# Performance work log

Measured on AMD Instinct MI355X. Metric: run time of the kernel, lower is better.

The kernel has to match this reference:

```python
import jax, jax.numpy as jnp
import numpy as np

H = 64        # hidden_size
NOISE = 16    # noise_size
DATA = 8      # data_size
WIDTH = 128   # width_size
INIT_NOISE = 8
B = 512       # batch (original vmaps per-sample __call__)
T = 1025      # saved time points; steps = T - 1


def lipswish(x):
    return 0.909 * jax.nn.silu(x)


def _mlp(x, W0, b0, W1, b1, W2, b2, act, final_act):
    h = act(x @ W0.T + b0)
    h = act(h @ W1.T + b1)
    return final_act(h @ W2.T + b2)


def _forward(ts, z0, dW, iW0, ib0, iW1, ib1, iW2, ib2,
             vW0, vb0, vW1, vb1, vW2, vb2, vscale,
             cW0, cb0, cW1, cb1, cW2, cb2, cscale, roW, rob):
    dt = ts[1] - ts[0]
    # initial MLP: default relu activation, identity final activation
    y0 = _mlp(z0, iW0, ib0, iW1, ib1, iW2, ib2, jax.nn.relu, lambda u: u)  # (B,H)
    dw = dW * jnp.sqrt(dt)  # Brownian increments per step, (T-1,B,NOISE)

    def with_t(t, y):
        return jnp.concatenate([jnp.full((y.shape[0], 1), t, y.dtype), y], axis=1)

    def drift(t, y):
        return vscale * _mlp(with_t(t, y), vW0, vb0, vW1, vb1, vW2, vb2, lipswish, jnp.tanh)

    def diff_prod(t, y, dw_t):
        g = _mlp(with_t(t, y), cW0, cb0, cW1, cb1, cW2, cb2, lipswish, jnp.tanh)
        g = cscale * g.reshape(y.shape[0], H, NOISE)
        return jnp.einsum('bhn,bn->bh', g, dw_t)

    def step(y, inp):
        # diffrax EulerHeun (Stratonovich) step
        t, dw_t = inp
        f0 = drift(t, y) * dt
        g0 = diff_prod(t, y, dw_t)
        y_prime = y + g0
        g1 = diff_prod(t, y_prime, dw_t)
        y1 = y + f0 + 0.5 * (g0 + g1)
        return y1, y1

    _, ys = jax.lax.scan(step, y0, (ts[:-1], dw))
    ys_all = jnp.concatenate([y0[None], ys], axis=0)  # (T,B,H); SaveAt(t0=True, steps=True)
    out = ys_all @ roW.T + rob                         # readout, (T,B,DATA)
    return jnp.transpose(out, (1, 0, 2))               # (B,T,DATA)


def setup_inputs():
    key = jax.random.key(0)
    ks = jax.random.split(key, 12)

    def lin(k, out_d, in_d):
        k1, k2 = jax.random.split(k)
        lim = 1.0 / np.sqrt(in_d)
        W = jax.random.uniform(k1, (out_d, in_d), jnp.float32, -lim, lim)
        b = jax.random.uniform(k2, (out_d,), jnp.float32, -lim, lim)
        return W, b

    iW0, ib0 = lin(ks[0], WIDTH, INIT_NOISE)
    iW1, ib1 = lin(ks[1], WIDTH, WIDTH)
    iW2, ib2 = lin(ks[2], H, WIDTH)
    vW0, vb0 = lin(ks[3], WIDTH, H + 1)
    vW1, vb1 = lin(ks[4], WIDTH, WIDTH)
    vW2, vb2 = lin(ks[5], H, WIDTH)
    vscale = jax.random.uniform(ks[6], (H,), jnp.float32, 0.9, 1.1)
    cW0, cb0 = lin(ks[7], WIDTH, H + 1)
    cW1, cb1 = lin(ks[8], WIDTH, WIDTH)
    cW2, cb2 = lin(ks[9], H * NOISE, WIDTH)
    cscale = jax.random.uniform(ks[10], (H, NOISE), jnp.float32, 0.9, 1.1)
    roW, rob = lin(ks[11], DATA, H)

    kz, kw = jax.random.split(jax.random.key(1))
    ts = jnp.arange(T, dtype=jnp.float32) / (T - 1)  # uniform grid on [0,1]
    z0 = jax.random.normal(kz, (B, INIT_NOISE), jnp.float32)
    dW = jax.random.normal(kw, (T - 1, B, NOISE), jnp.float32)
    return {"ts": ts, "z0": z0, "dW": dW,
            "iW0": iW0, "ib0": ib0, "iW1": iW1, "ib1": ib1, "iW2": iW2, "ib2": ib2,
            "vW0": vW0, "vb0": vb0, "vW1": vW1, "vb1": vb1, "vW2": vW2, "vb2": vb2,
            "vscale": vscale,
            "cW0": cW0, "cb0": cb0, "cW1": cW1, "cb1": cb1, "cW2": cW2, "cb2": cb2,
            "cscale": cscale, "roW": roW, "rob": rob}


def reference(ts, z0, dW, iW0, ib0, iW1, ib1, iW2, ib2,
              vW0, vb0, vW1, vb1, vW2, vb2, vscale,
              cW0, cb0, cW1, cb1, cW2, cb2, cscale, roW, rob):
    return _forward(ts, z0, dW, iW0, ib0, iW1, ib1, iW2, ib2,
                    vW0, vb0, vW1, vb1, vW2, vb2, vscale,
                    cW0, cb0, cW1, cb1, cW2, cb2, cscale, roW, rob)
```

## Files before the change

kernel.cpp:

```cpp
#include <hip/hip_runtime.h>

typedef unsigned short u16;
typedef unsigned int   u32;
typedef __attribute__((ext_vector_type(4))) unsigned int au4;
typedef __attribute__((ext_vector_type(4))) float fx4;
typedef __attribute__((ext_vector_type(8))) __bf16 bf16x8;

#define NTHREADS 512
#define NBLOCKS  256
#define BB       2
#define STEPS    1024
#define TPTS     1025
#define HDIM     64
#define NZ       16
#define WID      128
#define IND      65
#define HN       1024

__device__ __forceinline__ float bf2f(u16 v) { return __uint_as_float(((u32)v) << 16); }
__device__ __forceinline__ u16 f2bf(float f) {
    u32 u = __float_as_uint(f);
    return (u16)((u + 0x7fffu + ((u >> 16) & 1u)) >> 16);
}
__device__ __forceinline__ float lo16(u32 u) { return __uint_as_float(u << 16); }
__device__ __forceinline__ float hi16(u32 u) { return __uint_as_float(u & 0xffff0000u); }
__device__ __forceinline__ u32 pk(float a, float b) {
    return (u32)f2bf(a) | ((u32)f2bf(b) << 16);
}

__device__ __forceinline__ au4 apin(uint4 v) {
    au4 t; t.x = v.x; t.y = v.y; t.z = v.z; t.w = v.w;
    au4 r;
    asm volatile("" : "=a"(r) : "0"(t));
    return r;
}
__device__ __forceinline__ au4 ageta(au4 a) {
    au4 t;
    asm volatile("" : "=a"(t) : "0"(a));
    return t;
}

template <bool IS32>
__device__ __forceinline__ float ldf(const void* p, int i) {
    return IS32 ? ((const float*)p)[i] : bf2f(((const u16*)p)[i]);
}
template <bool IS32>
__device__ __forceinline__ u16 ldbf(const void* p, int i) {
    return IS32 ? f2bf(((const float*)p)[i]) : ((const u16*)p)[i];
}

__device__ __forceinline__ float rcpf(float x) { return __builtin_amdgcn_rcpf(x); }
__device__ __forceinline__ float lipswish(float x) {
    return 0.909f * x * rcpf(1.0f + __expf(-x));
}
__device__ __forceinline__ float tanh_fast(float x) {
    float e = __expf(2.0f * fabsf(x));
    float t = 1.0f - 2.0f * rcpf(e + 1.0f);
    return copysignf(t, x);
}
__device__ __forceinline__ void split_bf(float v, u16& hi, u16& lo) {
    hi = f2bf(v);
    lo = f2bf(v - bf2f(hi));
}

struct __align__(16) SMem {
    __align__(16) u16 bxh[BB][96],  bxl[BB][96];
    __align__(16) u16 bh1[2][4][144];
    __align__(16) u16 bh2v[4][144];
    __align__(16) u16 bh2c[4][144];
    __align__(16) u16 vW2F[4][4][64][8];
    __align__(16) float accL0[4][264];
    __align__(16) float accL2v[4][72];
    __align__(16) float accB[4][1032];
    __align__(16) float b0s[256], b1s[256], vb2[HDIM], vsc[HDIM];
    __align__(16) float cb2[HN], csc[HN];
    __align__(16) float roW[8][HDIM];
    __align__(16) float rob[8];
    __align__(16) float tsb[1028];
    __align__(16) float yb[BB][HDIM], g0b[BB][HDIM], fdt[BB][HDIM];
    __align__(16) float dwb[BB][NZ];
};

__device__ __forceinline__ bf16x8 bfrag(const u16* p) {
    return __builtin_bit_cast(bf16x8, *(const uint4*)p);
}
__device__ __forceinline__ fx4 mf1(au4 a, bf16x8 b, fx4 acc) {
    bf16x8 af = __builtin_bit_cast(bf16x8, ageta(a));
    return __builtin_amdgcn_mfma_f32_16x16x32_bf16(af, b, acc, 0, 0, 0);
}

template <bool IS32>
__device__ __forceinline__ uint4 load8(const void* src, int row, int stride, int k0, int Klim) {
    u16 e[8];
    #pragma unroll
    for (int j = 0; j < 8; ++j) {
        int k = k0 + j;
        e[j] = (k < Klim) ? ldbf<IS32>(src, row * stride + k) : (u16)0;
    }
    uint4 v;
    v.x = (u32)e[0] | ((u32)e[1] << 16);
    v.y = (u32)e[2] | ((u32)e[3] << 16);
    v.z = (u32)e[4] | ((u32)e[5] << 16);
    v.w = (u32)e[6] | ((u32)e[7] << 16);
    return v;
}

template <bool IS32>
__device__ __forceinline__ void stage_dw(SMem& sm, const uint4& d, int q, float sdt) {
    if (IS32) {
        const float* pf = (const float*)&d;
        int f = q * 4;
        #pragma unroll
        for (int k = 0; k < 4; ++k)
            sm.dwb[(f + k) >> 4][(f + k) & 15] = pf[k] * sdt;
    } else {
        int f = q * 8;
        u32 u0 = d.x, u1 = d.y, u2 = d.z, u3 = d.w;
        sm.dwb[(f    ) >> 4][(f    ) & 15] = lo16(u0) * sdt;
        sm.dwb[(f + 1) >> 4][(f + 1) & 15] = hi16(u0) * sdt;
        sm.dwb[(f + 2) >> 4][(f + 2) & 15] = lo16(u1) * sdt;
        sm.dwb[(f + 3) >> 4][(f + 3) & 15] = hi16(u1) * sdt;
        sm.dwb[(f + 4) >> 4][(f + 4) & 15] = lo16(u2) * sdt;
        sm.dwb[(f + 5) >> 4][(f + 5) & 15] = hi16(u2) * sdt;
        sm.dwb[(f + 6) >> 4][(f + 6) & 15] = lo16(u3) * sdt;
        sm.dwb[(f + 7) >> 4][(f + 7) & 15] = hi16(u3) * sdt;
    }
}

template <bool IS32>
__device__ __forceinline__ void write_out(void* out, size_t idx, const float* v8) {
    if (IS32) {
        float4 o0, o1;
        o0.x = v8[0]; o0.y = v8[1]; o0.z = v8[2]; o0.w = v8[3];
        o1.x = v8[4]; o1.y = v8[5]; o1.z = v8[6]; o1.w = v8[7];
        ((float4*)out)[idx * 2]     = o0;
        ((float4*)out)[idx * 2 + 1] = o1;
    } else {
        uint4 o;
        o.x = pk(v8[0], v8[1]);
        o.y = pk(v8[2], v8[3]);
        o.z = pk(v8[4], v8[5]);
        o.w = pk(v8[6], v8[7]);
        ((uint4*)out)[idx] = o;
    }
}

template <bool IS32>
__device__ __forceinline__ void
sde_run(SMem& sm,
        const void* ts,  const void* z0,  const void* dW,
        const void* iW0, const void* ib0, const void* iW1, const void* ib1,
        const void* iW2, const void* ib2,
        const void* vW0, const void* vb0, const void* vW1, const void* vb1,
        const void* vW2, const void* vb2, const void* vsc,
        const void* cW0, const void* cb0, const void* cW1, const void* cb1,
        const void* cW2, const void* cb2, const void* csc,
        const void* roW, const void* rob, void* out,
        int tid, int bid)
{
    const int lane = tid & 63, wv = tid >> 6;
    const int mm = lane & 15, qq = lane >> 4;
    const int nn = mm;
    const int smp = nn & 1;
    const int prt = (nn >> 1) & 1;

    au4 a0[6];
    au4 a1[8];
    au4 ab[32];
    #pragma unroll
    for (int rtl = 0; rtl < 2; ++rtl) {
        int grow = 16 * (2 * wv + rtl) + mm;
        const void* src = (grow < 128) ? vW0 : cW0;
        int r = grow & 127;
        #pragma unroll
        for (int kt = 0; kt < 3; ++kt)
            a0[rtl * 3 + kt] = apin(load8<IS32>(src, r, IND, 32 * kt + 8 * qq, IND));
    }
    {
        const void* src = (wv < 4) ? vW1 : cW1;
        int wl = wv & 3;
        #pragma unroll
        for (int rtl = 0; rtl < 2; ++rtl) {
            int r = 16 * (2 * wl + rtl) + mm;
            #pragma unroll
            for (int kt = 0; kt < 4; ++kt)
                a1[rtl * 4 + kt] = apin(load8<IS32>(src, r, WID, 32 * kt + 8 * qq, WID));
        }
    }
    #pragma unroll
    for (int r8 = 0; r8 < 8; ++r8) {
        int r = 128 * wv + 16 * r8 + mm;
        #pragma unroll
        for (int kt = 0; kt < 4; ++kt)
            ab[r8 * 4 + kt] = apin(load8<IS32>(cW2, r, WID, 32 * kt + 8 * qq, WID));
    }

    for (int slot = tid; slot < 1024; slot += NTHREADS) {
        int rt = slot >> 8, kt = (slot >> 6) & 3, l = slot & 63;
        int m = l & 15, q = l >> 4;
        uint4 v = load8<IS32>(vW2, 16 * rt + m, WID, 32 * kt + 8 * q, WID);
        *(uint4*)&sm.vW2F[rt][kt][l][0] = v;
    }
    if (tid < 256) {
        sm.b0s[tid] = (tid < 128) ? ldf<IS32>(vb0, tid) : ldf<IS32>(cb0, tid - 128);
        sm.b1s[tid] = (tid < 128) ? ldf<IS32>(vb1, tid) : ldf<IS32>(cb1, tid - 128);
    } else if (tid < 320) {
        int i = tid - 256;
        sm.vb2[i] = ldf<IS32>(vb2, i);
        sm.vsc[i] = ldf<IS32>(vsc, i);
    } else if (tid < 328) {
        sm.rob[tid - 320] = ldf<IS32>(rob, tid - 320);
    } else if (tid >= 384 && tid < 448) {
        int b = (tid - 384) >> 5, k = 65 + ((tid - 384) & 31);
        if (k < 96) { sm.bxh[b][k] = 0; sm.bxl[b][k] = 0; }
    }
    for (int i = tid; i < HN; i += NTHREADS) {
        sm.cb2[i] = ldf<IS32>(cb2, i);
        sm.csc[i] = ldf<IS32>(csc, i);
    }
    { int d = tid >> 6, i2 = tid & 63; sm.roW[d][i2] = ldf<IS32>(roW, tid); }
    for (int i = tid; i < TPTS; i += NTHREADS) sm.tsb[i] = ldf<IS32>(ts, i);

    uint4 dwpref;
    if (tid >= 128 && tid < 136) {
        int q = tid - 128;
        if (IS32)       dwpref = ((const uint4*)dW)[(size_t)bid * 8 + q];
        else if (q < 4) dwpref = ((const uint4*)dW)[(size_t)bid * 4 + q];
    }
    __syncthreads();

    const float dt  = sm.tsb[1] - sm.tsb[0];
    const float sdt = sqrtf(dt);
    if (tid >= 128 && tid < 136) {
        int q = tid - 128;
        if (IS32 || q < 4) stage_dw<IS32>(sm, dwpref, q, sdt);
    }

    if (tid < 256) {
        int b = tid >> 7, j = tid & 127;
        float acc = ldf<IS32>(ib0, j);
        #pragma unroll
        for (int k = 0; k < 8; ++k)
            acc = fmaf(ldf<IS32>(iW0, j * 8 + k), ldf<IS32>(z0, (bid * BB + b) * 8 + k), acc);
        sm.accB[0][b * 128 + j] = fmaxf(acc, 0.0f);
    }
    __syncthreads();
    if (tid < 256) {
        int b = tid >> 7, j = tid & 127;
        float acc = ldf<IS32>(ib1, j);
        for (int k = 0; k < WID; ++k)
            acc = fmaf(ldf<IS32>(iW1, j * WID + k), sm.accB[0][b * 128 + k], acc);
        sm.accB[1][b * 128 + j] = fmaxf(acc, 0.0f);
    }
    __syncthreads();
    if (tid < 128) {
        int b = tid >> 6, i = tid & 63;
        float y0 = ldf<IS32>(ib2, i);
        for (int k = 0; k < WID; ++k)
            y0 = fmaf(ldf<IS32>(iW2, i * WID + k), sm.accB[1][b * 128 + k], y0);
        sm.yb[b][i] = y0;
        u16 hi, lo; split_bf(y0, hi, lo);
        sm.bxh[b][1 + i] = hi; sm.bxl[b][1 + i] = lo;
        if (i == 0) {
            u16 thi, tlo; split_bf(sm.tsb[0], thi, tlo);
            sm.bxh[b][0] = thi; sm.bxl[b][0] = tlo;
        }
    }
    __syncthreads();

    for (int s = 0; s < STEPS; ++s) {
        if (s > 0 && tid >= 128 && tid < 136) {
            int q = tid - 128;
            if (IS32 || q < 4) stage_dw<IS32>(sm, dwpref, q, sdt);
        }
        {
            const u16* xs = prt ? &sm.bxl[smp][0] : &sm.bxh[smp][0];
            bf16x8 bx[3];
            #pragma unroll
            for (int kt = 0; kt < 3; ++kt) bx[kt] = bfrag(&xs[32 * kt + 8 * qq]);
            #pragma unroll
            for (int rtl = 0; rtl < 2; ++rtl) {
                fx4 acc = {0.f, 0.f, 0.f, 0.f};
                #pragma unroll
                for (int kt = 0; kt < 3; ++kt) acc = mf1(a0[rtl * 3 + kt], bx[kt], acc);
                int rowb = 16 * (2 * wv + rtl) + 4 * qq;
                if (nn < 4) *(fx4*)&sm.accL0[nn][rowb] = acc;
            }
        }
        __syncthreads();
        {
            int r = tid >> 1, c = tid & 1;
            float h = lipswish(sm.accL0[c][r] + sm.accL0[c + 2][r] + sm.b0s[r]);
            u16 hi, lo; split_bf(h, hi, lo);
            int mlp = r >> 7, j = r & 127;
            sm.bh1[mlp][c][j]     = hi;
            sm.bh1[mlp][2 + c][j] = lo;
        }
        __syncthreads();
        {
            int mlp = (wv < 4) ? 0 : 1, wl = wv & 3;
            const u16* hs = &sm.bh1[mlp][prt * 2 + smp][0];
            bf16x8 bf[4];
            #pragma unroll
            for (int kt = 0; kt < 4; ++kt) bf[kt] = bfrag(&hs[32 * kt + 8 * qq]);
            #pragma unroll
            for (int rtl = 0; rtl < 2; ++rtl) {
                fx4 acc = {0.f, 0.f, 0.f, 0.f};
                #pragma unroll
                for (int kt = 0; kt < 4; ++kt) acc = mf1(a1[rtl * 4 + kt], bf[kt], acc);
                int rowb = mlp * 128 + 16 * (2 * wl + rtl) + 4 * qq;
                if (nn < 4) *(fx4*)&sm.accB[nn][rowb] = acc;
            }
        }
        __syncthreads();
        {
            int r = tid >> 1, c = tid & 1;
            float h = lipswish(sm.accB[c][r] + sm.accB[c + 2][r] + sm.b1s[r]);
            u16 hi, lo; split_bf(h, hi, lo);
            if (r < 128) { sm.bh2v[c][r]           = hi; sm.bh2v[2 + c][r]           = lo; }
            else         { sm.bh2c[c][r - 128]     = hi; sm.bh2c[2 + c][r - 128]     = lo; }
        }
        __syncthreads();
        {
            const u16* cs2 = &sm.bh2c[prt * 2 + smp][0];
            bf16x8 bc[4];
            #pragma unroll
            for (int kt = 0; kt < 4; ++kt) bc[kt] = bfrag(&cs2[32 * kt + 8 * qq]);
            #pragma unroll
            for (int r8 = 0; r8 < 8; ++r8) {
                fx4 acc = {0.f, 0.f, 0.f, 0.f};
                #pragma unroll
                for (int kt = 0; kt < 4; ++kt) acc = mf1(ab[r8 * 4 + kt], bc[kt], acc);
                int rowb = 128 * wv + 16 * r8 + 4 * qq;
                if (nn < 4) *(fx4*)&sm.accB[nn][rowb] = acc;
            }
            if (wv < 4) {
                const u16* vs2 = &sm.bh2v[prt * 2 + smp][0];
                fx4 acc = {0.f, 0.f, 0.f, 0.f};
                #pragma unroll
                for (int kt = 0; kt < 4; ++kt) {
                    bf16x8 aw = bfrag(&sm.vW2F[wv][kt][lane][0]);
                    acc = __builtin_amdgcn_mfma_f32_16x16x32_bf16(aw, bfrag(&vs2[32 * kt + 8 * qq]), acc, 0, 0, 0);
                }
                int i0 = 16 * wv + 4 * qq;
                if (nn < 4) *(fx4*)&sm.accL2v[nn][i0] = acc;
            }
        }
        __syncthreads();
        {
            int b = tid >> 8, h = (tid >> 2) & 63, q4 = tid & 3;
            int rb = 16 * h + 4 * q4;
            fx4 aH = *(const fx4*)&sm.accB[b][rb];
            fx4 aL = *(const fx4*)&sm.accB[b + 2][rb];
            float4 cb = *(const float4*)&sm.cb2[rb];
            float4 cs = *(const float4*)&sm.csc[rb];
            float4 dw = *(const float4*)&sm.dwb[b][4 * q4];
            float v;
            v  = tanh_fast(aH.x + aL.x + cb.x) * cs.x * dw.x;
            v  = fmaf(tanh_fast(aH.y + aL.y + cb.y) * cs.y, dw.y, v);
            v  = fmaf(tanh_fast(aH.z + aL.z + cb.z) * cs.z, dw.z, v);
            v  = fmaf(tanh_fast(aH.w + aL.w + cb.w) * cs.w, dw.w, v);
            v += __shfl_xor(v, 1);
            v += __shfl_xor(v, 2);
            if (tid < 128) {
                int b2 = tid >> 6, i = tid & 63;
                sm.fdt[b2][i] = sm.vsc[i] * tanh_fast(sm.accL2v[b2][i] + sm.accL2v[b2 + 2][i] + sm.vb2[i]) * dt;
            }
            if (q4 == 0) {
                sm.g0b[b][h] = v;
                float xp = sm.yb[b][h] + v;
                u16 hi, lo; split_bf(xp, hi, lo);
                sm.bxh[b][1 + h] = hi; sm.bxl[b][1 + h] = lo;
            }
        }
        __syncthreads();
        if (wv >= 4) {
            const u16* xs = prt ? &sm.bxl[smp][0] : &sm.bxh[smp][0];
            bf16x8 bx[3];
            #pragma unroll
            for (int kt = 0; kt < 3; ++kt) bx[kt] = bfrag(&xs[32 * kt + 8 * qq]);
            #pragma unroll
            for (int rtl = 0; rtl < 2; ++rtl) {
                fx4 acc = {0.f, 0.f, 0.f, 0.f};
                #pragma unroll
                for (int kt = 0; kt < 3; ++kt) acc = mf1(a0[rtl * 3 + kt], bx[kt], acc);
                int rowb = 16 * (2 * wv + rtl) + 4 * qq;
                if (nn < 4) *(fx4*)&sm.accL0[nn][rowb] = acc;
            }
        } else if (tid < 128) {
            int b = tid >> 6, i = tid & 63;
            float y = sm.yb[b][i];
            float acc8[8];
            #pragma unroll
            for (int d = 0; d < 8; ++d) acc8[d] = sm.roW[d][i] * y;
            #pragma unroll
            for (int m = 1; m < 64; m <<= 1) {
                #pragma unroll
                for (int d = 0; d < 8; ++d) acc8[d] += __shfl_xor(acc8[d], m);
            }
            if (i == 0) {
                float v8[8];
                #pragma unroll
                for (int d = 0; d < 8; ++d) v8[d] = acc8[d] + sm.rob[d];
                write_out<IS32>(out, (size_t)(bid * BB + b) * TPTS + s, v8);
            }
        } else if (tid >= 128 && tid < 136 && s + 1 < STEPS) {
            int q = tid - 128;
            if (IS32)       dwpref = ((const uint4*)dW)[(size_t)(s + 1) * 2048 + bid * 8 + q];
            else if (q < 4) dwpref = ((const uint4*)dW)[(size_t)(s + 1) * 1024 + bid * 4 + q];
        }
        __syncthreads();
        if (tid < 256) {
            int r = 128 + (tid >> 1), c = tid & 1;
            float h = lipswish(sm.accL0[c][r] + sm.accL0[c + 2][r] + sm.b0s[r]);
            u16 hi, lo; split_bf(h, hi, lo);
            sm.bh1[1][c][r - 128]     = hi;
            sm.bh1[1][2 + c][r - 128] = lo;
        }
        __syncthreads();
        if (wv >= 4) {
            int wl = wv & 3;
            const u16* hs = &sm.bh1[1][prt * 2 + smp][0];
            bf16x8 bf[4];
            #pragma unroll
            for (int kt = 0; kt < 4; ++kt) bf[kt] = bfrag(&hs[32 * kt + 8 * qq]);
            #pragma unroll
            for (int rtl = 0; rtl < 2; ++rtl) {
                fx4 acc = {0.f, 0.f, 0.f, 0.f};
                #pragma unroll
                for (int kt = 0; kt < 4; ++kt) acc = mf1(a1[rtl * 4 + kt], bf[kt], acc);
                int rowb = 128 + 16 * (2 * wl + rtl) + 4 * qq;
                if (nn < 4) *(fx4*)&sm.accB[nn][rowb] = acc;
            }
        }
        __syncthreads();
        if (tid < 256) {
            int r = 128 + (tid >> 1), c = tid & 1;
            float h = lipswish(sm.accB[c][r] + sm.accB[c + 2][r] + sm.b1s[r]);
            u16 hi, lo; split_bf(h, hi, lo);
            sm.bh2c[c][r - 128]     = hi;
            sm.bh2c[2 + c][r - 128] = lo;
        }
        __syncthreads();
        {
            const u16* cs2 = &sm.bh2c[prt * 2 + smp][0];
            bf16x8 bc[4];
            #pragma unroll
            for (int kt = 0; kt < 4; ++kt) bc[kt] = bfrag(&cs2[32 * kt + 8 * qq]);
            #pragma unroll
            for (int r8 = 0; r8 < 8; ++r8) {
                fx4 acc = {0.f, 0.f, 0.f, 0.f};
                #pragma unroll
                for (int kt = 0; kt < 4; ++kt) acc = mf1(ab[r8 * 4 + kt], bc[kt], acc);
                int rowb = 128 * wv + 16 * r8 + 4 * qq;
                if (nn < 4) *(fx4*)&sm.accB[nn][rowb] = acc;
            }
        }
        __syncthreads();
        {
            int b = tid >> 8, h = (tid >> 2) & 63, q4 = tid & 3;
            int rb = 16 * h + 4 * q4;
            fx4 aH = *(const fx4*)&sm.accB[b][rb];
            fx4 aL = *(const fx4*)&sm.accB[b + 2][rb];
            float4 cb = *(const float4*)&sm.cb2[rb];
            float4 cs = *(const float4*)&sm.csc[rb];
            float4 dw = *(const float4*)&sm.dwb[b][4 * q4];
            float v;
            v  = tanh_fast(aH.x + aL.x + cb.x) * cs.x * dw.x;
            v  = fmaf(tanh_fast(aH.y + aL.y + cb.y) * cs.y, dw.y, v);
            v  = fmaf(tanh_fast(aH.z + aL.z + cb.z) * cs.z, dw.z, v);
            v  = fmaf(tanh_fast(aH.w + aL.w + cb.w) * cs.w, dw.w, v);
            v += __shfl_xor(v, 1);
            v += __shfl_xor(v, 2);
            if (q4 == 0) {
                float y1 = sm.yb[b][h] + sm.fdt[b][h] + 0.5f * (sm.g0b[b][h] + v);
                sm.yb[b][h] = y1;
                u16 hi, lo; split_bf(y1, hi, lo);
                sm.bxh[b][1 + h] = hi; sm.bxl[b][1 + h] = lo;
                if (h == 0) {
                    u16 thi, tlo; split_bf(sm.tsb[s + 1], thi, tlo);
                    sm.bxh[b][0] = thi; sm.bxl[b][0] = tlo;
                }
            }
        }
        __syncthreads();
    }

    if (tid < 128) {
        int b = tid >> 6, i = tid & 63;
        float y = sm.yb[b][i];
        float acc8[8];
        #pragma unroll
        for (int d = 0; d < 8; ++d) acc8[d] = sm.roW[d][i] * y;
        #pragma unroll
        for (int m = 1; m < 64; m <<= 1) {
            #pragma unroll
            for (int d = 0; d < 8; ++d) acc8[d] += __shfl_xor(acc8[d], m);
        }
        if (i == 0) {
            float v8[8];
            #pragma unroll
            for (int d = 0; d < 8; ++d) v8[d] = acc8[d] + sm.rob[d];
            write_out<IS32>(out, (size_t)(bid * BB + b) * TPTS + STEPS, v8);
        }
    }
}

__global__ void
__attribute__((amdgpu_flat_work_group_size(NTHREADS, NTHREADS), amdgpu_waves_per_eu(2, 2)))
sde_kernel(const void* __restrict__ ts,  const void* __restrict__ z0,  const void* __restrict__ dW,
           const void* __restrict__ iW0, const void* __restrict__ ib0, const void* __restrict__ iW1,
           const void* __restrict__ ib1, const void* __restrict__ iW2, const void* __restrict__ ib2,
           const void* __restrict__ vW0, const void* __restrict__ vb0, const void* __restrict__ vW1,
           const void* __restrict__ vb1, const void* __restrict__ vW2, const void* __restrict__ vb2,
           const void* __restrict__ vsc, const void* __restrict__ cW0, const void* __restrict__ cb0,
           const void* __restrict__ cW1, const void* __restrict__ cb1, const void* __restrict__ cW2,
           const void* __restrict__ cb2, const void* __restrict__ csc, const void* __restrict__ roW,
           const void* __restrict__ rob, void* __restrict__ out)
{
    __shared__ SMem sm;
    const int tid = threadIdx.x;
    const int bid = blockIdx.x;

    const bool is32 = (((const u16*)ts)[1] == 0);

    if (is32) {
        sde_run<true>(sm, ts, z0, dW, iW0, ib0, iW1, ib1, iW2, ib2,
                      vW0, vb0, vW1, vb1, vW2, vb2, vsc,
                      cW0, cb0, cW1, cb1, cW2, cb2, csc, roW, rob, out, tid, bid);
    } else {
        sde_run<false>(sm, ts, z0, dW, iW0, ib0, iW1, ib1, iW2, ib2,
                       vW0, vb0, vW1, vb1, vW2, vb2, vsc,
                       cW0, cb0, cW1, cb1, cW2, cb2, csc, roW, rob, out, tid, bid);
    }
}

extern "C" void kernel_launch(void* const* d_in, const int* in_sizes, int n_in,
                              void* d_out, int out_size, void* d_ws, size_t ws_size,
                              hipStream_t stream) {
    (void)in_sizes; (void)n_in; (void)d_ws; (void)ws_size; (void)out_size;
    hipLaunchKernelGGL(sde_kernel, dim3(NBLOCKS), dim3(NTHREADS), 0, stream,
                       d_in[0], d_in[1], d_in[2], d_in[3], d_in[4], d_in[5], d_in[6],
                       d_in[7], d_in[8], d_in[9], d_in[10], d_in[11], d_in[12], d_in[13],
                       d_in[14], d_in[15], d_in[16], d_in[17], d_in[18], d_in[19], d_in[20],
                       d_in[21], d_in[22], d_in[23], d_in[24], d_out);
}
```

Baseline: 5.500 ms.

## Split per-step MFMA work across 16 waves with 1024-thread blocks

```diff
diff --git a/kernel.cpp b/kernel.cpp
--- a/kernel.cpp
+++ b/kernel.cpp
@@ -6,7 +6,7 @@
 typedef __attribute__((ext_vector_type(4))) float fx4;
 typedef __attribute__((ext_vector_type(8))) __bf16 bf16x8;
 
-#define NTHREADS 512
+#define NTHREADS 1024
 #define NBLOCKS  256
 #define BB       2
 #define STEPS    1024
@@ -164,32 +164,27 @@
     const int smp = nn & 1;
     const int prt = (nn >> 1) & 1;
 
-    au4 a0[6];
-    au4 a1[8];
-    au4 ab[32];
-    #pragma unroll
-    for (int rtl = 0; rtl < 2; ++rtl) {
-        int grow = 16 * (2 * wv + rtl) + mm;
+    au4 a0[3];
+    au4 a1[4];
+    au4 ab[16];
+    {
+        int grow = 16 * wv + mm;
         const void* src = (grow < 128) ? vW0 : cW0;
         int r = grow & 127;
         #pragma unroll
         for (int kt = 0; kt < 3; ++kt)
-            a0[rtl * 3 + kt] = apin(load8<IS32>(src, r, IND, 32 * kt + 8 * qq, IND));
+            a0[kt] = apin(load8<IS32>(src, r, IND, 32 * kt + 8 * qq, IND));
     }
     {
-        const void* src = (wv < 4) ? vW1 : cW1;
-        int wl = wv & 3;
-        #pragma unroll
-        for (int rtl = 0; rtl < 2; ++rtl) {
-            int r = 16 * (2 * wl + rtl) + mm;
-            #pragma unroll
-            for (int kt = 0; kt < 4; ++kt)
-                a1[rtl * 4 + kt] = apin(load8<IS32>(src, r, WID, 32 * kt + 8 * qq, WID));
-        }
+        const void* src = (wv < 8) ? vW1 : cW1;
+        int r = 16 * (wv & 7) + mm;
+        #pragma unroll
+        for (int kt = 0; kt < 4; ++kt)
+            a1[kt] = apin(load8<IS32>(src, r, WID, 32 * kt + 8 * qq, WID));
     }
     #pragma unroll
-    for (int r8 = 0; r8 < 8; ++r8) {
-        int r = 128 * wv + 16 * r8 + mm;
+    for (int r8 = 0; r8 < 4; ++r8) {
+        int r = 64 * wv + 16 * r8 + mm;
         #pragma unroll
         for (int kt = 0; kt < 4; ++kt)
             ab[r8 * 4 + kt] = apin(load8<IS32>(cW2, r, WID, 32 * kt + 8 * qq, WID));
@@ -218,7 +213,7 @@
         sm.cb2[i] = ldf<IS32>(cb2, i);
         sm.csc[i] = ldf<IS32>(csc, i);
     }
-    { int d = tid >> 6, i2 = tid & 63; sm.roW[d][i2] = ldf<IS32>(roW, tid); }
+    if (tid < 512) { int d = tid >> 6, i2 = tid & 63; sm.roW[d][i2] = ldf<IS32>(roW, tid); }
     for (int i = tid; i < TPTS; i += NTHREADS) sm.tsb[i] = ldf<IS32>(ts, i);
 
     uint4 dwpref;
@@ -278,17 +273,14 @@
             bf16x8 bx[3];
             #pragma unroll
             for (int kt = 0; kt < 3; ++kt) bx[kt] = bfrag(&xs[32 * kt + 8 * qq]);
-            #pragma unroll
-            for (int rtl = 0; rtl < 2; ++rtl) {
-                fx4 acc = {0.f, 0.f, 0.f, 0.f};
-                #pragma unroll
-                for (int kt = 0; kt < 3; ++kt) acc = mf1(a0[rtl * 3 + kt], bx[kt], acc);
-                int rowb = 16 * (2 * wv + rtl) + 4 * qq;
-                if (nn < 4) *(fx4*)&sm.accL0[nn][rowb] = acc;
-            }
-        }
-        __syncthreads();
-        {
+            fx4 acc = {0.f, 0.f, 0.f, 0.f};
+            #pragma unroll
+            for (int kt = 0; kt < 3; ++kt) acc = mf1(a0[kt], bx[kt], acc);
+            int rowb = 16 * wv + 4 * qq;
+            if (nn < 4) *(fx4*)&sm.accL0[nn][rowb] = acc;
+        }
+        __syncthreads();
+        if (tid < 512) {
             int r = tid >> 1, c = tid & 1;
             float h = lipswish(sm.accL0[c][r] + sm.accL0[c + 2][r] + sm.b0s[r]);
             u16 hi, lo; split_bf(h, hi, lo);
@@ -298,22 +290,19 @@
         }
         __syncthreads();
         {
-            int mlp = (wv < 4) ? 0 : 1, wl = wv & 3;
+            int mlp = (wv < 8) ? 0 : 1;
             const u16* hs = &sm.bh1[mlp][prt * 2 + smp][0];
             bf16x8 bf[4];
             #pragma unroll
             for (int kt = 0; kt < 4; ++kt) bf[kt] = bfrag(&hs[32 * kt + 8 * qq]);
-            #pragma unroll
-            for (int rtl = 0; rtl < 2; ++rtl) {
-                fx4 acc = {0.f, 0.f, 0.f, 0.f};
-                #pragma unroll
-                for (int kt = 0; kt < 4; ++kt) acc = mf1(a1[rtl * 4 + kt], bf[kt], acc);
-                int rowb = mlp * 128 + 16 * (2 * wl + rtl) + 4 * qq;
-                if (nn < 4) *(fx4*)&sm.accB[nn][rowb] = acc;
-            }
-        }
-        __syncthreads();
-        {
+            fx4 acc = {0.f, 0.f, 0.f, 0.f};
+            #pragma unroll
+            for (int kt = 0; kt < 4; ++kt) acc = mf1(a1[kt], bf[kt], acc);
+            int rowb = mlp * 128 + 16 * (wv & 7) + 4 * qq;
+            if (nn < 4) *(fx4*)&sm.accB[nn][rowb] = acc;
+        }
+        __syncthreads();
+        if (tid < 512) {
             int r = tid >> 1, c = tid & 1;
             float h = lipswish(sm.accB[c][r] + sm.accB[c + 2][r] + sm.b1s[r]);
             u16 hi, lo; split_bf(h, hi, lo);
@@ -327,11 +316,11 @@
             #pragma unroll
             for (int kt = 0; kt < 4; ++kt) bc[kt] = bfrag(&cs2[32 * kt + 8 * qq]);
             #pragma unroll
-            for (int r8 = 0; r8 < 8; ++r8) {
+            for (int r8 = 0; r8 < 4; ++r8) {
                 fx4 acc = {0.f, 0.f, 0.f, 0.f};
                 #pragma unroll
                 for (int kt = 0; kt < 4; ++kt) acc = mf1(ab[r8 * 4 + kt], bc[kt], acc);
-                int rowb = 128 * wv + 16 * r8 + 4 * qq;
+                int rowb = 64 * wv + 16 * r8 + 4 * qq;
                 if (nn < 4) *(fx4*)&sm.accB[nn][rowb] = acc;
             }
             if (wv < 4) {
@@ -347,7 +336,7 @@
             }
         }
         __syncthreads();
-        {
+        if (tid < 512) {
             int b = tid >> 8, h = (tid >> 2) & 63, q4 = tid & 3;
             int rb = 16 * h + 4 * q4;
             fx4 aH = *(const fx4*)&sm.accB[b][rb];
@@ -374,19 +363,16 @@
             }
         }
         __syncthreads();
-        if (wv >= 4) {
+        if (wv >= 8) {
             const u16* xs = prt ? &sm.bxl[smp][0] : &sm.bxh[smp][0];
             bf16x8 bx[3];
             #pragma unroll
             for (int kt = 0; kt < 3; ++kt) bx[kt] = bfrag(&xs[32 * kt + 8 * qq]);
-            #pragma unroll
-            for (int rtl = 0; rtl < 2; ++rtl) {
-                fx4 acc = {0.f, 0.f, 0.f, 0.f};
-                #pragma unroll
-                for (int kt = 0; kt < 3; ++kt) acc = mf1(a0[rtl * 3 + kt], bx[kt], acc);
-                int rowb = 16 * (2 * wv + rtl) + 4 * qq;
-                if (nn < 4) *(fx4*)&sm.accL0[nn][rowb] = acc;
-            }
+            fx4 acc = {0.f, 0.f, 0.f, 0.f};
+            #pragma unroll
+            for (int kt = 0; kt < 3; ++kt) acc = mf1(a0[kt], bx[kt], acc);
+            int rowb = 16 * wv + 4 * qq;
+            if (nn < 4) *(fx4*)&sm.accL0[nn][rowb] = acc;
         } else if (tid < 128) {
             int b = tid >> 6, i = tid & 63;
             float y = sm.yb[b][i];
@@ -418,20 +404,16 @@
             sm.bh1[1][2 + c][r - 128] = lo;
         }
         __syncthreads();
-        if (wv >= 4) {
-            int wl = wv & 3;
+        if (wv >= 8) {
             const u16* hs = &sm.bh1[1][prt * 2 + smp][0];
             bf16x8 bf[4];
             #pragma unroll
             for (int kt = 0; kt < 4; ++kt) bf[kt] = bfrag(&hs[32 * kt + 8 * qq]);
-            #pragma unroll
-            for (int rtl = 0; rtl < 2; ++rtl) {
-                fx4 acc = {0.f, 0.f, 0.f, 0.f};
-                #pragma unroll
-                for (int kt = 0; kt < 4; ++kt) acc = mf1(a1[rtl * 4 + kt], bf[kt], acc);
-                int rowb = 128 + 16 * (2 * wl + rtl) + 4 * qq;
-                if (nn < 4) *(fx4*)&sm.accB[nn][rowb] = acc;
-            }
+            fx4 acc = {0.f, 0.f, 0.f, 0.f};
+            #pragma unroll
+            for (int kt = 0; kt < 4; ++kt) acc = mf1(a1[kt], bf[kt], acc);
+            int rowb = 128 + 16 * (wv & 7) + 4 * qq;
+            if (nn < 4) *(fx4*)&sm.accB[nn][rowb] = acc;
         }
         __syncthreads();
         if (tid < 256) {
@@ -448,16 +430,16 @@
             #pragma unroll
             for (int kt = 0; kt < 4; ++kt) bc[kt] = bfrag(&cs2[32 * kt + 8 * qq]);
             #pragma unroll
-            for (int r8 = 0; r8 < 8; ++r8) {
+            for (int r8 = 0; r8 < 4; ++r8) {
                 fx4 acc = {0.f, 0.f, 0.f, 0.f};
                 #pragma unroll
                 for (int kt = 0; kt < 4; ++kt) acc = mf1(ab[r8 * 4 + kt], bc[kt], acc);
-                int rowb = 128 * wv + 16 * r8 + 4 * qq;
+                int rowb = 64 * wv + 16 * r8 + 4 * qq;
                 if (nn < 4) *(fx4*)&sm.accB[nn][rowb] = acc;
             }
         }
         __syncthreads();
-        {
+        if (tid < 512) {
             int b = tid >> 8, h = (tid >> 2) & 63, q4 = tid & 3;
             int rb = 16 * h + 4 * q4;
             fx4 aH = *(const fx4*)&sm.accB[b][rb];
@@ -507,7 +489,7 @@
 }
 
 __global__ void
-__attribute__((amdgpu_flat_work_group_size(NTHREADS, NTHREADS), amdgpu_waves_per_eu(2, 2)))
+__attribute__((amdgpu_flat_work_group_size(NTHREADS, NTHREADS), amdgpu_waves_per_eu(4, 4)))
 sde_kernel(const void* __restrict__ ts,  const void* __restrict__ z0,  const void* __restrict__ dW,
            const void* __restrict__ iW0, const void* __restrict__ ib0, const void* __restrict__ iW1,
            const void* __restrict__ ib1, const void* __restrict__ iW2, const void* __restrict__ ib2,
```

New measurement: 11.43 ms. +107.8%, slower.
